# Optimization experiments

Measured on AMD Instinct MI355X. Metric: run time of the kernel, lower is better.

## Reference

```python
import jax, jax.numpy as jnp
import numpy as np

H, DH, C = 16, 64, 1024  # num_head, head_size, embed_size
B, T = 4, 2048

def setup_inputs() -> dict:
    key = jax.random.key(0)
    ks = jax.random.split(key, 6)
    s = 1.0 / np.sqrt(C)
    x  = jax.random.normal(ks[0], (B, T, C), dtype=jnp.float32)
    # per-head projection weights, stacked: [H, C, DH] (PyTorch Linear computes x @ W.T; we store W.T directly)
    Wq = jax.random.uniform(ks[1], (H, C, DH), dtype=jnp.float32, minval=-s, maxval=s)
    Wk = jax.random.uniform(ks[2], (H, C, DH), dtype=jnp.float32, minval=-s, maxval=s)
    Wv = jax.random.uniform(ks[3], (H, C, DH), dtype=jnp.float32, minval=-s, maxval=s)
    Wo = jax.random.uniform(ks[4], (C, C), dtype=jnp.float32, minval=-s, maxval=s)
    bo = jax.random.uniform(ks[5], (C,), dtype=jnp.float32, minval=-s, maxval=s)
    return {"x": x, "Wq": Wq, "Wk": Wk, "Wv": Wv, "Wo": Wo, "bo": bo}

def reference(x, Wq, Wk, Wv, Wo, bo):
    # Dropout layers act as identity (eval mode).
    q = jnp.einsum('btc,hcd->bhtd', x, Wq)
    k = jnp.einsum('btc,hcd->bhtd', x, Wk)
    v = jnp.einsum('btc,hcd->bhtd', x, Wv)
    scale = 1.0 / np.sqrt(DH).astype(np.float32)
    wei = jnp.einsum('bhtd,bhsd->bhts', q, k) * scale  # [B,H,T,T]
    Tn = x.shape[1]
    causal = jnp.tril(jnp.ones((Tn, Tn), dtype=bool))
    wei = jnp.where(causal, wei, -jnp.inf)
    wei = jax.nn.softmax(wei, axis=-1)
    out = jnp.einsum('bhts,bhsd->bhtd', wei, v)  # [B,H,T,DH]
    out = out.transpose(0, 2, 1, 3).reshape(x.shape[0], Tn, H * DH)  # concat heads
    return out @ Wo + bo
```

## Files before the change

kernel.cpp:

```cpp
#include <hip/hip_runtime.h>
#include <hip/hip_bf16.h>

typedef __attribute__((ext_vector_type(8))) short short8;
typedef __attribute__((ext_vector_type(4))) short s4v;
typedef __attribute__((ext_vector_type(4))) float floatx4;
typedef __attribute__((ext_vector_type(4))) unsigned int u32x4;

static constexpr int Hn = 16, DHn = 64, Cn = 1024;
static constexpr int Bn = 4, Tn = 2048;
static constexpr int Mtot = Bn * Tn;
static constexpr size_t QKV_STRIDE = (size_t)Bn * Hn * Tn * DHn;

__device__ __forceinline__ unsigned short bfbits(float f) {
    __hip_bfloat16 h = __float2bfloat16(f);
    return __builtin_bit_cast(unsigned short, h);
}

__device__ __forceinline__ unsigned int cvtpk(float a, float b) {
    unsigned int r;
    asm("v_cvt_pk_bf16_f32 %0, %1, %2" : "=v"(r) : "v"(a), "v"(b));
    return r;
}

__device__ __forceinline__ void gl_lds16(const void* g, void* lds_base) {
    __builtin_amdgcn_global_load_lds(
        (const __attribute__((address_space(1))) unsigned int*)g,
        (__attribute__((address_space(3))) unsigned int*)lds_base, 16, 0, 0);
}

__global__ void conv_kernel(const float4* __restrict__ src, ushort4* __restrict__ dst, int n4) {
    int i = blockIdx.x * blockDim.x + threadIdx.x;
    if (i < n4) {
        float4 v = src[i];
        ushort4 o;
        o.x = bfbits(v.x); o.y = bfbits(v.y); o.z = bfbits(v.z); o.w = bfbits(v.w);
        dst[i] = o;
    }
}

__global__ void tconv_kernel(const float* __restrict__ src, __hip_bfloat16* __restrict__ dst,
                             int R, int C, float scale) {
    __shared__ float tile[32][33];
    const float* s = src + (size_t)blockIdx.z * R * C;
    __hip_bfloat16* d = dst + (size_t)blockIdx.z * R * C;
    int c0 = blockIdx.x * 32;
    int r0 = blockIdx.y * 32;
    int tx = threadIdx.x;
    int ty = threadIdx.y;
    for (int i = 0; i < 4; ++i) {
        int r = r0 + ty + i * 8;
        tile[ty + i * 8][tx] = s[(size_t)r * C + c0 + tx];
    }
    __syncthreads();
    for (int i = 0; i < 4; ++i) {
        int c = c0 + ty + i * 8;
        d[(size_t)c * R + r0 + tx] = __float2bfloat16(tile[tx][ty + i * 8] * scale);
    }
}

template<int MODE>
__global__ __launch_bounds__(256) void gemm_kernel(
    const __hip_bfloat16* __restrict__ A,
    const __hip_bfloat16* __restrict__ BT,
    const float* __restrict__ bias,
    __hip_bfloat16* __restrict__ out_qkv,
    float* __restrict__ out_f32)
{
    constexpr int K = Cn;
    constexpr int NSTEP = K / 64;
    __shared__ char smem[65536];

    const int m0 = blockIdx.x * 128;
    const int n0 = blockIdx.y * 128;

    const int tid = threadIdx.x;
    const int lane = tid & 63, wid = tid >> 6;
    const int wy = wid >> 1, wx = wid & 1;
    const int fr = lane & 15, g = lane >> 4;
    const int rxor = (fr & 7) << 4;

    floatx4 acc[4][4] = {};

    int srow[4], scol[4], doff[4];
#pragma unroll
    for (int i = 0; i < 4; ++i) {
        int byteoff = wid * 4096 + i * 1024 + lane * 16;
        int r = byteoff >> 7;
        int ch = (byteoff >> 4) & 7;
        srow[i] = r;
        scol[i] = (ch ^ (r & 7)) << 3;
        doff[i] = wid * 4096 + i * 1024;
    }

#pragma unroll
    for (int i = 0; i < 4; ++i) {
        gl_lds16(&A[(size_t)(m0 + srow[i]) * K + scol[i]], smem + doff[i]);
        gl_lds16(&BT[(size_t)(n0 + srow[i]) * K + scol[i]], smem + 16384 + doff[i]);
    }
    asm volatile("s_waitcnt vmcnt(0)" ::: "memory");
    asm volatile("s_barrier" ::: "memory");

    int cur = 0;
    for (int t = 0; t < NSTEP; ++t) {
        if (t + 1 < NSTEP) {
            const int k0 = (t + 1) * 64;
            char* dst = smem + (cur ^ 1) * 32768;
#pragma unroll
            for (int i = 0; i < 4; ++i) {
                gl_lds16(&A[(size_t)(m0 + srow[i]) * K + k0 + scol[i]], dst + doff[i]);
                gl_lds16(&BT[(size_t)(n0 + srow[i]) * K + k0 + scol[i]], dst + 16384 + doff[i]);
            }
        }
        const char* lA0 = smem + cur * 32768;
        const char* lB0 = lA0 + 16384;
#pragma unroll
        for (int kk = 0; kk < 2; ++kk) {
            short8 af[4], bf[4];
#pragma unroll
            for (int t4 = 0; t4 < 4; ++t4) {
                af[t4] = *(const short8*)(lA0 + (wy * 64 + t4 * 16 + fr) * 128 + ((kk * 64 + g * 16) ^ rxor));
                bf[t4] = *(const short8*)(lB0 + (wx * 64 + t4 * 16 + fr) * 128 + ((kk * 64 + g * 16) ^ rxor));
            }
            __builtin_amdgcn_s_setprio(1);
#pragma unroll
            for (int tm = 0; tm < 4; ++tm)
#pragma unroll
                for (int tn = 0; tn < 4; ++tn)
                    acc[tm][tn] = __builtin_amdgcn_mfma_f32_16x16x32_bf16(af[tm], bf[tn], acc[tm][tn], 0, 0, 0);
            __builtin_amdgcn_s_setprio(0);
        }
        asm volatile("s_waitcnt vmcnt(0)" ::: "memory");
        asm volatile("s_barrier" ::: "memory");
        cur ^= 1;
    }

    for (int tm = 0; tm < 4; ++tm) {
        int rbase = m0 + wy * 64 + tm * 16 + g * 4;
        for (int tn = 0; tn < 4; ++tn) {
            int nc = n0 + wx * 64 + tn * 16 + fr;
            if (MODE == 0) {
                int w = nc >> 10, rem = nc & 1023, hh = rem >> 6, dd = rem & 63;
                if (w == 2) {
                    int b = rbase >> 11, t0 = rbase & 2047;
                    ushort4 pk;
                    pk.x = bfbits(acc[tm][tn][0]);
                    pk.y = bfbits(acc[tm][tn][1]);
                    pk.z = bfbits(acc[tm][tn][2]);
                    pk.w = bfbits(acc[tm][tn][3]);
                    *(ushort4*)(&out_qkv[2 * QKV_STRIDE +
                        ((size_t)((b * Hn + hh) * DHn + dd)) * Tn + t0]) = pk;
                } else {
                    for (int r = 0; r < 4; ++r) {
                        int m = rbase + r;
                        int b = m >> 11, t = m & 2047;
                        out_qkv[(size_t)w * QKV_STRIDE + (((size_t)(b * Hn + hh) * Tn + t) << 6) + dd] =
                            __float2bfloat16(acc[tm][tn][r]);
                    }
                }
            } else {
                float bs = bias[nc];
                for (int r = 0; r < 4; ++r) {
                    int m = rbase + r;
                    out_f32[(size_t)m * Cn + nc] = acc[tm][tn][r] + bs;
                }
            }
        }
    }
}

__global__ __launch_bounds__(256, 4) void attn_kernel(
    const __hip_bfloat16* __restrict__ q,
    const __hip_bfloat16* __restrict__ k,
    const __hip_bfloat16* __restrict__ vt,
    __hip_bfloat16* __restrict__ ao)
{
    __shared__ char smem[32768];

    const int id = blockIdx.x;
    const int xcd = id & 7;
    const int rnk = id >> 3;
    const int tile = 15 - (rnk >> 3);
    const int bh = xcd * 8 + (rnk & 7);
    const int b = bh >> 4, h = bh & 15;
    const int tid = threadIdx.x, lane = tid & 63, wid = tid >> 6;
    const int fr = lane & 15, g = lane >> 4;
    const size_t base = (size_t)bh * Tn * DHn;
    const int rxor = (fr & 7) << 4;

    const int r0 = wid * 16 + (lane >> 3);
    const int c8 = ((lane & 7) ^ (r0 & 7)) * 8;
    const int ldk0 = wid * 2048;

    short8 ones;
#pragma unroll
    for (int z = 0; z < 8; ++z) ones[z] = (short)0x3F80;

    const int qb0 = tile * 128;
    const int q0 = qb0 + wid * 32;
    const int nkv = qb0 / 64 + 2;

    short8 aq[2][2];
#pragma unroll
    for (int rq = 0; rq < 2; ++rq)
#pragma unroll
        for (int kk = 0; kk < 2; ++kk)
            aq[rq][kk] = *(const short8*)(&q[base + (size_t)(q0 + rq * 16 + fr) * DHn + kk * 32 + g * 8]);

    floatx4 o[2][4] = {};
    floatx4 o5[2] = {};

    {
        char* kd = smem + ldk0;
        char* vd = smem + 16384 + ldk0;
        gl_lds16(&k[base + (size_t)r0 * DHn + c8], kd);
        gl_lds16(&k[base + (size_t)(r0 + 8) * DHn + c8], kd + 1024);
        gl_lds16(&vt[base + (size_t)r0 * Tn + c8], vd);
        gl_lds16(&vt[base + (size_t)(r0 + 8) * Tn + c8], vd + 1024);
    }
    asm volatile("s_waitcnt vmcnt(0)" ::: "memory");
    __builtin_amdgcn_s_barrier();

    int cur = 0;
    for (int j = 0; j < nkv; ++j) {
        const int kv0 = j * 64;

        {
            const int nv0 = kv0 + 64;
            char* kd = smem + (cur ^ 1) * 8192 + ldk0;
            char* vd = smem + 16384 + (cur ^ 1) * 8192 + ldk0;
            gl_lds16(&k[base + (size_t)(nv0 + r0) * DHn + c8], kd);
            gl_lds16(&k[base + (size_t)(nv0 + r0 + 8) * DHn + c8], kd + 1024);
            gl_lds16(&vt[base + (size_t)r0 * Tn + nv0 + c8], vd);
            gl_lds16(&vt[base + (size_t)(r0 + 8) * Tn + nv0 + c8], vd + 1024);
        }

        if (kv0 < q0 + 32) {
            const char* lkc = smem + cur * 8192;
            const char* lvc = smem + 16384 + cur * 8192;

            floatx4 s[2][4] = {};
            __builtin_amdgcn_s_setprio(1);
#pragma unroll
            for (int kk = 0; kk < 2; ++kk)
#pragma unroll
                for (int cg = 0; cg < 4; ++cg) {
                    short8 kf = *(const short8*)(lkc + (cg * 16 + fr) * 128 + ((g * 16 + kk * 64) ^ rxor));
                    s[0][cg] = __builtin_amdgcn_mfma_f32_16x16x32_bf16(kf, aq[0][kk], s[0][cg], 0, 0, 0);
                    s[1][cg] = __builtin_amdgcn_mfma_f32_16x16x32_bf16(kf, aq[1][kk], s[1][cg], 0, 0, 0);
                }
            __builtin_amdgcn_s_setprio(0);

            if (kv0 + 64 > q0) {
#pragma unroll
                for (int rq = 0; rq < 2; ++rq) {
                    int qg = q0 + rq * 16 + fr;
#pragma unroll
                    for (int cg = 0; cg < 4; ++cg) {
                        int kg = kv0 + cg * 16 + g * 4;
#pragma unroll
                        for (int r = 0; r < 4; ++r)
                            if (kg + r > qg) s[rq][cg][r] = -1e30f;
                    }
                }
            }

            short8 pb[2][2];
#pragma unroll
            for (int rq = 0; rq < 2; ++rq) {
#pragma unroll
                for (int cg = 0; cg < 4; ++cg)
#pragma unroll
                    for (int r = 0; r < 4; ++r)
                        s[rq][cg][r] = __builtin_amdgcn_exp2f(s[rq][cg][r]);
#pragma unroll
                for (int kt = 0; kt < 2; ++kt) {
                    u32x4 wv;
                    wv[0] = cvtpk(s[rq][2 * kt][0],     s[rq][2 * kt][1]);
                    wv[1] = cvtpk(s[rq][2 * kt][2],     s[rq][2 * kt][3]);
                    wv[2] = cvtpk(s[rq][2 * kt + 1][0], s[rq][2 * kt + 1][1]);
                    wv[3] = cvtpk(s[rq][2 * kt + 1][2], s[rq][2 * kt + 1][3]);
                    pb[rq][kt] = __builtin_bit_cast(short8, wv);
                }
            }

            __builtin_amdgcn_s_setprio(1);
#pragma unroll
            for (int rq = 0; rq < 2; ++rq)
#pragma unroll
                for (int kt = 0; kt < 2; ++kt)
                    o5[rq] = __builtin_amdgcn_mfma_f32_16x16x32_bf16(ones, pb[rq][kt], o5[rq], 0, 0, 0);
#pragma unroll
            for (int kt = 0; kt < 2; ++kt)
#pragma unroll
                for (int dg = 0; dg < 4; ++dg) {
                    const int vrow = (dg * 16 + fr) * 128;
                    s4v lo = *(const s4v*)(lvc + vrow + ((kt * 64 + 8 * g) ^ rxor));
                    s4v hi = *(const s4v*)(lvc + vrow + ((kt * 64 + 32 + 8 * g) ^ rxor));
                    short8 vf = __builtin_shufflevector(lo, hi, 0, 1, 2, 3, 4, 5, 6, 7);
                    o[0][dg] = __builtin_amdgcn_mfma_f32_16x16x32_bf16(vf, pb[0][kt], o[0][dg], 0, 0, 0);
                    o[1][dg] = __builtin_amdgcn_mfma_f32_16x16x32_bf16(vf, pb[1][kt], o[1][dg], 0, 0, 0);
                }
            __builtin_amdgcn_s_setprio(0);
        }

        asm volatile("s_waitcnt vmcnt(0)" ::: "memory");
        __builtin_amdgcn_s_barrier();
        cur ^= 1;
    }

    char* myscr = smem + wid * 4096;
    const int rr = lane >> 2, cc = lane & 3;
#pragma unroll
    for (int rq = 0; rq < 2; ++rq) {
        const float inv = 1.0f / o5[rq][0];
#pragma unroll
        for (int dg = 0; dg < 4; ++dg) {
            floatx4 wv = o[rq][dg] * inv;
            *(floatx4*)(myscr + fr * 256 + ((dg * 64 + g * 16) ^ rxor)) = wv;
        }
        asm volatile("s_waitcnt lgkmcnt(0)" ::: "memory");
        float4 f0 = *(const float4*)(myscr + rr * 256 + ((cc * 64 + 0) ^ ((rr & 7) << 4)));
        float4 f1 = *(const float4*)(myscr + rr * 256 + ((cc * 64 + 16) ^ ((rr & 7) << 4)));
        float4 f2 = *(const float4*)(myscr + rr * 256 + ((cc * 64 + 32) ^ ((rr & 7) << 4)));
        float4 f3 = *(const float4*)(myscr + rr * 256 + ((cc * 64 + 48) ^ ((rr & 7) << 4)));
        short8 pk0, pk1;
        pk0[0] = (short)bfbits(f0.x); pk0[1] = (short)bfbits(f0.y);
        pk0[2] = (short)bfbits(f0.z); pk0[3] = (short)bfbits(f0.w);
        pk0[4] = (short)bfbits(f1.x); pk0[5] = (short)bfbits(f1.y);
        pk0[6] = (short)bfbits(f1.z); pk0[7] = (short)bfbits(f1.w);
        pk1[0] = (short)bfbits(f2.x); pk1[1] = (short)bfbits(f2.y);
        pk1[2] = (short)bfbits(f2.z); pk1[3] = (short)bfbits(f2.w);
        pk1[4] = (short)bfbits(f3.x); pk1[5] = (short)bfbits(f3.y);
        pk1[6] = (short)bfbits(f3.z); pk1[7] = (short)bfbits(f3.w);
        size_t orow = ((size_t)(b * Tn + q0 + rq * 16 + rr)) * Cn + h * 64 + cc * 16;
        *(short8*)(&ao[orow]) = pk0;
        *(short8*)(&ao[orow + 8]) = pk1;
        asm volatile("s_waitcnt lgkmcnt(0)" ::: "memory");
    }
}

extern "C" void kernel_launch(void* const* d_in, const int* in_sizes, int n_in,
                              void* d_out, int out_size, void* d_ws, size_t ws_size,
                              hipStream_t stream) {
    const float* x  = (const float*)d_in[0];
    const float* Wq = (const float*)d_in[1];
    const float* Wk = (const float*)d_in[2];
    const float* Wv = (const float*)d_in[3];
    const float* Wo = (const float*)d_in[4];
    const float* bo = (const float*)d_in[5];
    float* out = (float*)d_out;

    char* ws = (char*)d_ws;
    __hip_bfloat16* xb  = (__hip_bfloat16*)(ws);
    __hip_bfloat16* wT  = (__hip_bfloat16*)(ws + 16777216);
    __hip_bfloat16* woT = (__hip_bfloat16*)(ws + 23068672);
    __hip_bfloat16* qb  = (__hip_bfloat16*)(ws + 25165824);
    __hip_bfloat16* ao  = (__hip_bfloat16*)(ws + 75497472);

    conv_kernel<<<(Mtot * Cn / 4 + 255) / 256, 256, 0, stream>>>(
        (const float4*)x, (ushort4*)xb, Mtot * Cn / 4);
    tconv_kernel<<<dim3(2, 32, 16), dim3(32, 8), 0, stream>>>(Wq, wT + 0 * 1048576, Cn, DHn, 0.125f * 1.44269504088896f);
    tconv_kernel<<<dim3(2, 32, 16), dim3(32, 8), 0, stream>>>(Wk, wT + 1 * 1048576, Cn, DHn, 1.0f);
    tconv_kernel<<<dim3(2, 32, 16), dim3(32, 8), 0, stream>>>(Wv, wT + 2 * 1048576, Cn, DHn, 1.0f);
    tconv_kernel<<<dim3(32, 32, 1), dim3(32, 8), 0, stream>>>(Wo, woT, Cn, Cn, 1.0f);

    gemm_kernel<0><<<dim3(Mtot / 128, 3072 / 128), 256, 0, stream>>>(
        xb, wT, nullptr, qb, nullptr);

    attn_kernel<<<dim3(1024), 256, 0, stream>>>(
        qb, qb + QKV_STRIDE, qb + 2 * QKV_STRIDE, ao);

    gemm_kernel<1><<<dim3(Mtot / 128, Cn / 128), 256, 0, stream>>>(
        ao, woT, bo, nullptr, out);
}
```

Measured before the change: 146.1 us.

## Use 4-stage LDS ring with 32-wide K tiles and prefetch depth two in GEMM

The GEMM main loop moves from a double-buffered 64-wide K step to a four-buffer ring of 32-wide K tiles. Global-to-LDS loads are issued two tiles ahead, and the wait uses a partial vmcnt so only the oldest loads must finish. This keeps more memory traffic in flight and removes the trailing barrier each iteration. The cost is twice as many iterations and barriers per K, a new XOR swizzle for the narrower rows, and redundant reloads of the last tile near the end.

```diff
diff --git a/kernel.cpp b/kernel.cpp
--- a/kernel.cpp
+++ b/kernel.cpp
@@ -67,7 +67,7 @@
     float* __restrict__ out_f32)
 {
     constexpr int K = Cn;
-    constexpr int NSTEP = K / 64;
+    constexpr int NSTEP = K / 32;
     __shared__ char smem[65536];
 
     const int m0 = blockIdx.x * 128;
@@ -77,62 +77,52 @@
     const int lane = tid & 63, wid = tid >> 6;
     const int wy = wid >> 1, wx = wid & 1;
     const int fr = lane & 15, g = lane >> 4;
-    const int rxor = (fr & 7) << 4;
 
     floatx4 acc[4][4] = {};
 
-    int srow[4], scol[4], doff[4];
-#pragma unroll
-    for (int i = 0; i < 4; ++i) {
-        int byteoff = wid * 4096 + i * 1024 + lane * 16;
-        int r = byteoff >> 7;
-        int ch = (byteoff >> 4) & 7;
-        srow[i] = r;
-        scol[i] = (ch ^ (r & 7)) << 3;
-        doff[i] = wid * 4096 + i * 1024;
-    }
-
-#pragma unroll
-    for (int i = 0; i < 4; ++i) {
-        gl_lds16(&A[(size_t)(m0 + srow[i]) * K + scol[i]], smem + doff[i]);
-        gl_lds16(&BT[(size_t)(n0 + srow[i]) * K + scol[i]], smem + 16384 + doff[i]);
-    }
-    asm volatile("s_waitcnt vmcnt(0)" ::: "memory");
-    asm volatile("s_barrier" ::: "memory");
-
-    int cur = 0;
+    const int srow = wid * 32 + (lane >> 2);
+    const int scol = ((lane & 3) ^ ((lane >> 2) & 3)) * 8;
+    const int ldoff = wid * 2048;
+
+    const int rchk = (g ^ (fr & 3)) * 16;
+
+#define STAGE_G(tile, buf)                                                            \
+    {                                                                                 \
+        const int k0s = (tile) * 32;                                                  \
+        char* da = smem + (buf) * 8192 + ldoff;                                       \
+        char* db = smem + 32768 + (buf) * 8192 + ldoff;                               \
+        gl_lds16(&A[(size_t)(m0 + srow) * K + k0s + scol], da);                       \
+        gl_lds16(&A[(size_t)(m0 + srow + 16) * K + k0s + scol], da + 1024);           \
+        gl_lds16(&BT[(size_t)(n0 + srow) * K + k0s + scol], db);                      \
+        gl_lds16(&BT[(size_t)(n0 + srow + 16) * K + k0s + scol], db + 1024);          \
+    }
+
+    STAGE_G(0, 0);
+    STAGE_G(1, 1);
+
     for (int t = 0; t < NSTEP; ++t) {
-        if (t + 1 < NSTEP) {
-            const int k0 = (t + 1) * 64;
-            char* dst = smem + (cur ^ 1) * 32768;
-#pragma unroll
-            for (int i = 0; i < 4; ++i) {
-                gl_lds16(&A[(size_t)(m0 + srow[i]) * K + k0 + scol[i]], dst + doff[i]);
-                gl_lds16(&BT[(size_t)(n0 + srow[i]) * K + k0 + scol[i]], dst + 16384 + doff[i]);
-            }
-        }
-        const char* lA0 = smem + cur * 32768;
-        const char* lB0 = lA0 + 16384;
-#pragma unroll
-        for (int kk = 0; kk < 2; ++kk) {
-            short8 af[4], bf[4];
-#pragma unroll
-            for (int t4 = 0; t4 < 4; ++t4) {
-                af[t4] = *(const short8*)(lA0 + (wy * 64 + t4 * 16 + fr) * 128 + ((kk * 64 + g * 16) ^ rxor));
-                bf[t4] = *(const short8*)(lB0 + (wx * 64 + t4 * 16 + fr) * 128 + ((kk * 64 + g * 16) ^ rxor));
-            }
-            __builtin_amdgcn_s_setprio(1);
-#pragma unroll
-            for (int tm = 0; tm < 4; ++tm)
-#pragma unroll
-                for (int tn = 0; tn < 4; ++tn)
-                    acc[tm][tn] = __builtin_amdgcn_mfma_f32_16x16x32_bf16(af[tm], bf[tn], acc[tm][tn], 0, 0, 0);
-            __builtin_amdgcn_s_setprio(0);
-        }
-        asm volatile("s_waitcnt vmcnt(0)" ::: "memory");
-        asm volatile("s_barrier" ::: "memory");
-        cur ^= 1;
-    }
+        int nt = t + 2; if (nt > NSTEP - 1) nt = NSTEP - 1;
+        STAGE_G(nt, (t + 2) & 3);
+        asm volatile("s_waitcnt vmcnt(8)" ::: "memory");
+        __builtin_amdgcn_s_barrier();
+
+        const char* lA0 = smem + (t & 3) * 8192;
+        const char* lB0 = smem + 32768 + (t & 3) * 8192;
+        short8 af[4], bf[4];
+#pragma unroll
+        for (int t4 = 0; t4 < 4; ++t4) {
+            af[t4] = *(const short8*)(lA0 + (wy * 64 + t4 * 16 + fr) * 64 + rchk);
+            bf[t4] = *(const short8*)(lB0 + (wx * 64 + t4 * 16 + fr) * 64 + rchk);
+        }
+        __builtin_amdgcn_s_setprio(1);
+#pragma unroll
+        for (int tm = 0; tm < 4; ++tm)
+#pragma unroll
+            for (int tn = 0; tn < 4; ++tn)
+                acc[tm][tn] = __builtin_amdgcn_mfma_f32_16x16x32_bf16(af[tm], bf[tn], acc[tm][tn], 0, 0, 0);
+        __builtin_amdgcn_s_setprio(0);
+    }
+#undef STAGE_G
 
     for (int tm = 0; tm < 4; ++tm) {
         int rbase = m0 + wy * 64 + tm * 16 + g * 4;
```

After: 158.7 us. +8.6%, slower.
